# Performance work log

Hardware: AMD Instinct MI355X
Metric: run time of the kernel (lower is better)

Reference implementation:

```python
import jax, jax.numpy as jnp
import numpy as np

B = 2
H, W = 128, 128           # branch-0 map_size (target of all scatters)
N0 = 16384                # original grid points = H*W
IN_CH = [64, 128, 256, 512]
NS = [16384, 4096, 1024, 256]
OUT_C = 256
BN_EPS = 1e-5


def setup_inputs() -> dict:
    key = jax.random.key(0)
    ks = jax.random.split(key, 16)
    inp = {}
    for j, (c, n) in enumerate(zip(IN_CH, NS)):
        inp[f"x{j}"] = jax.random.normal(ks[4 * j], (B, n, c), jnp.float32)
        # grid_sample-style coords in [-1, 1]
        inp[f"loc{j}"] = jax.random.uniform(ks[4 * j + 1], (B, N0, 2), jnp.float32) * 2.0 - 1.0
        inp[f"idx{j}"] = jax.random.randint(ks[4 * j + 2], (B, N0), 0, n, dtype=jnp.int32)
        fan_out = 3 * 3 * OUT_C
        inp[f"w{j}"] = jax.random.normal(ks[4 * j + 3], (OUT_C, c, 3, 3), jnp.float32) * np.sqrt(2.0 / fan_out)
        inp[f"gamma{j}"] = jnp.ones((OUT_C,), jnp.float32)
        inp[f"beta{j}"] = jnp.zeros((OUT_C,), jnp.float32)
    return inp


def token2map(x, loc_orig, idx_agg):
    """Scatter-average token features x [B,N,C] onto a dense [B,C,H,W] map.
    Each of N0 original points carries the feature of its token (idx_agg) and
    lands in the grid cell given by loc_orig; cells average their points."""
    Bb, N, C = x.shape
    n0 = loc_orig.shape[1]
    loc = (jnp.clip(loc_orig, -1.0, 1.0) + 1.0) * 0.5
    ix = jnp.clip(jnp.round(loc[..., 0] * (W - 1)).astype(jnp.int32), 0, W - 1)
    iy = jnp.clip(jnp.round(loc[..., 1] * (H - 1)).astype(jnp.int32), 0, H - 1)
    cell = (ix + iy * W + jnp.arange(Bb, dtype=jnp.int32)[:, None] * (H * W)).reshape(-1)  # [B*N0]
    feat = jnp.take_along_axis(x, idx_agg[..., None], axis=1).reshape(Bb * n0, C)  # [B*N0, C]
    ones = jnp.ones((Bb * n0,), x.dtype)
    cnt = jax.ops.segment_sum(ones, cell, num_segments=Bb * H * W) + 1e-6  # points per cell
    val = (1.0 / cnt)[cell]  # per-point normalized weight
    out = jax.ops.segment_sum(feat * val[:, None], cell, num_segments=Bb * H * W)
    return out.reshape(Bb, H, W, C).transpose(0, 3, 1, 2)  # NCHW


def conv_bn(x, w, gamma, beta):
    # 3x3 stride-2 conv (bias=False) + BatchNorm2d (training mode: batch stats, biased var)
    y = jax.lax.conv_general_dilated(x, w, (2, 2), [(1, 1), (1, 1)],
                                     dimension_numbers=('NCHW', 'OIHW', 'NCHW'))
    mean = y.mean(axis=(0, 2, 3))
    var = y.var(axis=(0, 2, 3))
    y = (y - mean[None, :, None, None]) * jax.lax.rsqrt(var + BN_EPS)[None, :, None, None]
    return y * gamma[None, :, None, None] + beta[None, :, None, None]


def reference(x0, x1, x2, x3, loc0, loc1, loc2, loc3, idx0, idx1, idx2, idx3,
              w0, w1, w2, w3, gamma0, gamma1, gamma2, gamma3,
              beta0, beta1, beta2, beta3):
    xs = [x0, x1, x2, x3]
    locs = [loc0, loc1, loc2, loc3]
    idxs = [idx0, idx1, idx2, idx3]
    ws = [w0, w1, w2, w3]
    gs = [gamma0, gamma1, gamma2, gamma3]
    bs = [beta0, beta1, beta2, beta3]
    out_map = 0.0
    for j in range(4):  # fixed small loop over branches (structurally distinct C_j)
        m = token2map(xs[j], locs[j], idxs[j])
        out_map = out_map + conv_bn(m, ws[j], gs[j], bs[j])
    return out_map  # [B, 256, 64, 64]
```

## Files before the change

### kernel.cpp

```cpp
#include <hip/hip_runtime.h>

#define B 2
#define N0 16384
#define HW 16384
#define PADW 130
#define OUTC 256
#define M_ROWS 8192
#define MAXP 32

typedef short s16x8 __attribute__((ext_vector_type(8)));
typedef float f32x4 __attribute__((ext_vector_type(4)));

__device__ __forceinline__ unsigned short f2bf(float f) {
    union { float f; unsigned int u; } v; v.f = f;
    unsigned int u = v.u;
    return (unsigned short)((u + 0x7fffu + ((u >> 16) & 1u)) >> 16);
}
__device__ __forceinline__ float bf2f(unsigned short h) {
    union { unsigned int u; float f; } v; v.u = ((unsigned int)h) << 16;
    return v.f;
}

__device__ __forceinline__ void gl_lds16(const void* g, void* l) {
    __builtin_amdgcn_global_load_lds(
        (const __attribute__((address_space(1))) unsigned int*)g,
        (__attribute__((address_space(3))) unsigned int*)l, 16, 0, 0);
}

__device__ __forceinline__ void cell_of(const float* __restrict__ loc, int r, int& ix, int& iy) {
    float lx = loc[r * 2 + 0];
    float ly = loc[r * 2 + 1];
    lx = fminf(fmaxf(lx, -1.f), 1.f);
    ly = fminf(fmaxf(ly, -1.f), 1.f);
    ix = min(max((int)rintf(((lx + 1.f) * 0.5f) * 127.f), 0), 127);
    iy = min(max((int)rintf(((ly + 1.f) * 0.5f) * 127.f), 0), 127);
}

__global__ void fill_k(const float* __restrict__ l0, const float* __restrict__ l1,
                       const float* __restrict__ l2, const float* __restrict__ l3,
                       const int* __restrict__ i0, const int* __restrict__ i1,
                       const int* __restrict__ i2, const int* __restrict__ i3,
                       int* __restrict__ cnt32, unsigned short* __restrict__ list) {
    int p = blockIdx.x * 256 + threadIdx.x;
    int j = p >> 15, r = p & 32767;
    const float* loc = j == 0 ? l0 : j == 1 ? l1 : j == 2 ? l2 : l3;
    const int* idx = j == 0 ? i0 : j == 1 ? i1 : j == 2 ? i2 : i3;
    int ix, iy;
    cell_of(loc, r, ix, iy);
    int cidx = (((j << 1) + (r >> 14)) << 14) + iy * 128 + ix;
    int pos = atomicAdd(&cnt32[cidx], 1);
    if (pos < MAXP) list[cidx * MAXP + pos] = (unsigned short)idx[r];
}

__global__ void prep_k(const float* __restrict__ x0, const float* __restrict__ x1,
                       const float* __restrict__ x2, const float* __restrict__ x3,
                       const int* __restrict__ cnt32, const unsigned short* __restrict__ list,
                       unsigned short* __restrict__ mapB,
                       const float* __restrict__ w0, const float* __restrict__ w1,
                       const float* __restrict__ w2, const float* __restrict__ w3,
                       unsigned short* __restrict__ wt) {
    if (blockIdx.x >= 15844) {
        int i = (blockIdx.x - 15844) * 256 + threadIdx.x;
        if (i >= 2211840) return;
        int j, local;
        if (i < 147456) { j = 0; local = i; }
        else if (i < 442368) { j = 1; local = i - 147456; }
        else if (i < 1032192) { j = 2; local = i - 442368; }
        else { j = 3; local = i - 1032192; }
        const float* w = j == 0 ? w0 : j == 1 ? w1 : j == 2 ? w2 : w3;
        int lc = 6 + j, C = 1 << lc;
        int ci = local & (C - 1);
        int rest = local >> lc;
        int seg = rest % 9, co = rest / 9;
        int kh = seg / 3, kw = seg % 3;
        wt[(size_t)2304 * (C - 64) + local] = f2bf(w[(((co * C) + ci) * 3 + kh) * 3 + kw]);
        return;
    }
    int W = (blockIdx.x * 256 + threadIdx.x) >> 6;
    if (W >= 63375) return;
    int lane = threadIdx.x & 63;
    int j, base;
    if (W < 4225) { j = 0; base = 0; }
    else if (W < 12675) { j = 1; base = 4225; }
    else if (W < 29575) { j = 2; base = 12675; }
    else { j = 3; base = 29575; }
    const float* x = j == 0 ? x0 : j == 1 ? x1 : j == 2 ? x2 : x3;
    const int C = 64 << j;
    const int ntok = 16384 >> (2 * j);
    int u = W - base;
    int cellLocal = (u << (3 - j)) + (lane >> (3 + j));
    int sub = lane & ((8 << j) - 1);
    int ch0 = sub * 8;
    int b = cellLocal / 16900;
    int cc = cellLocal - b * 16900;
    int py = cc / 130, px = cc - py * 130;
    unsigned short* dst = mapB + (size_t)33800 * (C - 64) + ((size_t)cellLocal * C) + ch0;
    float a0 = 0.f, a1 = 0.f, a2 = 0.f, a3 = 0.f, a4 = 0.f, a5 = 0.f, a6 = 0.f, a7 = 0.f;
    if (py >= 1 && py <= 128 && px >= 1 && px <= 128) {
        int cidx = (((j << 1) + b) << 14) + (py - 1) * 128 + (px - 1);
        int n = cnt32[cidx];
        float inv = 1.0f / ((float)n + 1e-6f);
        int nn = min(n, MAXP);
        const unsigned short* lst = list + (size_t)cidx * MAXP;
        for (int p = 0; p < nn; p++) {
            int tok = lst[p];
            const float* xr = x + ((size_t)b * ntok + tok) * C + ch0;
            float4 v0 = *(const float4*)xr;
            float4 v1 = *(const float4*)(xr + 4);
            a0 += v0.x; a1 += v0.y; a2 += v0.z; a3 += v0.w;
            a4 += v1.x; a5 += v1.y; a6 += v1.z; a7 += v1.w;
        }
        a0 *= inv; a1 *= inv; a2 *= inv; a3 *= inv;
        a4 *= inv; a5 *= inv; a6 *= inv; a7 *= inv;
    }
    uint4 o;
    o.x = (unsigned int)f2bf(a0) | ((unsigned int)f2bf(a1) << 16);
    o.y = (unsigned int)f2bf(a2) | ((unsigned int)f2bf(a3) << 16);
    o.z = (unsigned int)f2bf(a4) | ((unsigned int)f2bf(a5) << 16);
    o.w = (unsigned int)f2bf(a6) | ((unsigned int)f2bf(a7) << 16);
    *(uint4*)dst = o;
}

__global__ __launch_bounds__(128) void conv_mfma(const unsigned short* __restrict__ mapB,
                                                 const unsigned short* __restrict__ wt,
                                                 unsigned short* __restrict__ P) {
    __shared__ unsigned short As[2][128][32];
    __shared__ unsigned short Bs[2][128][32];
    const int t = threadIdx.x;
    const int lane = t & 63;
    const int w = t >> 6;
    const int z = blockIdx.z;
    const int j = (z < 4) ? 3 : (z < 6) ? 2 : (z == 6) ? 1 : 0;
    const int lc = 6 + j;
    const int C = 1 << lc;
    const int K = 9 * C;
    const int s0 = (z < 4) ? z * 36 : (z == 5 ? 36 : 0);
    const int s1 = s0 + (j == 0 ? 18 : 36);
    const unsigned short* mapBj = mapB + (size_t)33800 * (C - 64);
    const unsigned short* wtj = wt + (size_t)2304 * (C - 64);
    unsigned short* Pz = P + (size_t)z * M_ROWS * OUTC;
    const int mt = blockIdx.x, nt = blockIdx.y;

    const int lr = lane >> 2, lq = lane & 3;
    const unsigned short* pA[4];
    const unsigned short* pB[4];
#pragma unroll
    for (int i = 0; i < 4; i++) {
        int r = w * 64 + i * 16 + lr;
        int s = mt * 128 + r;
        int b = s >> 12, rem = s & 4095, oh = rem >> 6, ow = rem & 63;
        pA[i] = mapBj + (size_t)((b * PADW + 2 * oh) * PADW + 2 * ow) * C + lq * 8;
        pB[i] = wtj + (size_t)(nt * 128 + r) * K + lq * 8;
    }

    int k0 = s0 << 5;
    int seg0 = k0 >> lc;
    int ci0 = k0 & (C - 1);
    int kh = seg0 / 3, kw = seg0 - 3 * kh;
    int offA = (kh * PADW + kw) * C + ci0;
    int offB = k0;

#pragma unroll
    for (int i = 0; i < 4; i++) {
        gl_lds16(pA[i] + offA, &As[0][w * 64 + i * 16][0]);
        gl_lds16(pB[i] + offB, &Bs[0][w * 64 + i * 16][0]);
    }

    f32x4 acc[8][4];
#pragma unroll
    for (int mi = 0; mi < 8; mi++)
#pragma unroll
        for (int ni = 0; ni < 4; ni++) acc[mi][ni] = (f32x4){0.f, 0.f, 0.f, 0.f};

    const int r16 = lane & 15, kg = lane >> 4;
    int buf = 0;
    for (int s = s0; s < s1; s++) {
        ci0 += 32; offA += 32; offB += 32;
        if (ci0 == C) {
            ci0 = 0; kw++;
            if (kw == 3) { kw = 0; offA += (PADW - 3) * C; }
        }
        __syncthreads();
        if (s + 1 < s1) {
            int nb = buf ^ 1;
#pragma unroll
            for (int i = 0; i < 4; i++) {
                gl_lds16(pA[i] + offA, &As[nb][w * 64 + i * 16][0]);
                gl_lds16(pB[i] + offB, &Bs[nb][w * 64 + i * 16][0]);
            }
        }
        s16x8 a[8], b[4];
#pragma unroll
        for (int mi = 0; mi < 8; mi++) a[mi] = *(const s16x8*)&As[buf][mi * 16 + r16][kg * 8];
#pragma unroll
        for (int ni = 0; ni < 4; ni++)
            b[ni] = *(const s16x8*)&Bs[buf][w * 64 + ni * 16 + r16][kg * 8];
#pragma unroll
        for (int mi = 0; mi < 8; mi++)
#pragma unroll
            for (int ni = 0; ni < 4; ni++)
                acc[mi][ni] = __builtin_amdgcn_mfma_f32_16x16x32_bf16(a[mi], b[ni],
                                                                      acc[mi][ni], 0, 0, 0);
        buf ^= 1;
    }

    const int rg = lane >> 4, c16 = lane & 15;
#pragma unroll
    for (int mi = 0; mi < 8; mi++)
#pragma unroll
        for (int ni = 0; ni < 4; ni++)
#pragma unroll
            for (int reg = 0; reg < 4; reg++) {
                int row = mt * 128 + mi * 16 + rg * 4 + reg;
                int col = nt * 128 + w * 64 + ni * 16 + c16;
                Pz[(size_t)row * OUTC + col] = f2bf(acc[mi][ni][reg]);
            }
}

__global__ void combine_k(const unsigned short* __restrict__ P,
                          unsigned short* __restrict__ ybr, float* __restrict__ branchAcc) {
    __shared__ float red_s[8][256], red_ss[8][256];
    int bi = blockIdx.x;
    int t = threadIdx.x;
    int cg = t & 31, rt = t >> 5;
    float s[4][8], ss[4][8];
#pragma unroll
    for (int j = 0; j < 4; j++)
#pragma unroll
        for (int k = 0; k < 8; k++) { s[j][k] = 0.f; ss[j][k] = 0.f; }
    for (int r = rt; r < 64; r += 8) {
        size_t row = (size_t)bi * 64 + r;
        const unsigned short* p = P + row * OUTC + cg * 8;
        float v[4][8];
#pragma unroll
        for (int j = 0; j < 4; j++)
#pragma unroll
            for (int k = 0; k < 8; k++) v[j][k] = 0.f;
#pragma unroll
        for (int z = 0; z < 8; z++) {
            int j = (z < 4) ? 3 : (z < 6) ? 2 : (z == 6) ? 1 : 0;
            uint4 u = *(const uint4*)(p + (size_t)z * M_ROWS * OUTC);
            v[j][0] += bf2f((unsigned short)(u.x & 0xffff));
            v[j][1] += bf2f((unsigned short)(u.x >> 16));
            v[j][2] += bf2f((unsigned short)(u.y & 0xffff));
            v[j][3] += bf2f((unsigned short)(u.y >> 16));
            v[j][4] += bf2f((unsigned short)(u.z & 0xffff));
            v[j][5] += bf2f((unsigned short)(u.z >> 16));
            v[j][6] += bf2f((unsigned short)(u.w & 0xffff));
            v[j][7] += bf2f((unsigned short)(u.w >> 16));
        }
#pragma unroll
        for (int j = 0; j < 4; j++) {
            uint4 o;
            o.x = (unsigned int)f2bf(v[j][0]) | ((unsigned int)f2bf(v[j][1]) << 16);
            o.y = (unsigned int)f2bf(v[j][2]) | ((unsigned int)f2bf(v[j][3]) << 16);
            o.z = (unsigned int)f2bf(v[j][4]) | ((unsigned int)f2bf(v[j][5]) << 16);
            o.w = (unsigned int)f2bf(v[j][6]) | ((unsigned int)f2bf(v[j][7]) << 16);
            *(uint4*)(ybr + ((size_t)j * M_ROWS + row) * OUTC + cg * 8) = o;
#pragma unroll
            for (int k = 0; k < 8; k++) {
                s[j][k] += v[j][k];
                ss[j][k] += v[j][k] * v[j][k];
            }
        }
    }
    for (int j = 0; j < 4; j++) {
#pragma unroll
        for (int k = 0; k < 8; k++) {
            red_s[rt][cg * 8 + k] = s[j][k];
            red_ss[rt][cg * 8 + k] = ss[j][k];
        }
        __syncthreads();
        float S = 0.f, SS = 0.f;
#pragma unroll
        for (int r = 0; r < 8; r++) { S += red_s[r][t]; SS += red_ss[r][t]; }
        atomicAdd(&branchAcc[j * 512 + t], S);
        atomicAdd(&branchAcc[j * 512 + 256 + t], SS);
        __syncthreads();
    }
}

__global__ void stats2_k(const float* __restrict__ branchAcc,
                         const float* __restrict__ g0, const float* __restrict__ g1,
                         const float* __restrict__ g2, const float* __restrict__ g3,
                         const float* __restrict__ b0, const float* __restrict__ b1,
                         const float* __restrict__ b2, const float* __restrict__ b3,
                         float* __restrict__ ssb) {
    int j = blockIdx.x, c = threadIdx.x;
    const float* gamma = j == 0 ? g0 : j == 1 ? g1 : j == 2 ? g2 : g3;
    const float* beta = j == 0 ? b0 : j == 1 ? b1 : j == 2 ? b2 : b3;
    float s = branchAcc[j * 512 + c];
    float ss = branchAcc[j * 512 + 256 + c];
    float mean = s * (1.f / 8192.f);
    float var = ss * (1.f / 8192.f) - mean * mean;
    float rs = rsqrtf(var + 1e-5f);
    float sc = gamma[c] * rs;
    ssb[j * 512 + c] = sc;
    ssb[j * 512 + OUTC + c] = beta[c] - mean * sc;
}

__global__ void out_k(const unsigned short* __restrict__ ybr, const float* __restrict__ ssb,
                      float* __restrict__ out) {
    __shared__ float tile[64][132];
    int oh = blockIdx.x, ct = blockIdx.y, b = blockIdx.z;
    int t = threadIdx.x;
    int cg = t & 31, rt = t >> 5;
    int c0 = ct * 128 + cg * 4;
    float sc[4][4], sh[4];
#pragma unroll
    for (int k = 0; k < 4; k++) {
        float shk = 0.f;
#pragma unroll
        for (int jj = 0; jj < 4; jj++) {
            sc[jj][k] = ssb[jj * 512 + c0 + k];
            shk += ssb[jj * 512 + OUTC + c0 + k];
        }
        sh[k] = shk;
    }
#pragma unroll
    for (int it = 0; it < 8; it++) {
        int ow = rt * 8 + it;
        size_t row = (size_t)b * 4096 + oh * 64 + ow;
        const unsigned short* p = ybr + row * OUTC + c0;
        float acc[4];
#pragma unroll
        for (int k = 0; k < 4; k++) acc[k] = sh[k];
#pragma unroll
        for (int jj = 0; jj < 4; jj++) {
            ushort4 u = *(const ushort4*)(p + (size_t)jj * M_ROWS * OUTC);
            acc[0] += bf2f(u.x) * sc[jj][0];
            acc[1] += bf2f(u.y) * sc[jj][1];
            acc[2] += bf2f(u.z) * sc[jj][2];
            acc[3] += bf2f(u.w) * sc[jj][3];
        }
#pragma unroll
        for (int k = 0; k < 4; k++) tile[ow][cg * 4 + k] = acc[k];
    }
    __syncthreads();
    int owq = t & 15, cp = t >> 4;
#pragma unroll
    for (int pass = 0; pass < 8; pass++) {
        int c = pass * 16 + cp;
        float4 v;
        v.x = tile[owq * 4 + 0][c];
        v.y = tile[owq * 4 + 1][c];
        v.z = tile[owq * 4 + 2][c];
        v.w = tile[owq * 4 + 3][c];
        *(float4*)(out + (((size_t)b * OUTC + ct * 128 + c) * 64 + oh) * 64 + owq * 4) = v;
    }
}

extern "C" void kernel_launch(void* const* d_in, const int* in_sizes, int n_in,
                              void* d_out, int out_size, void* d_ws, size_t ws_size,
                              hipStream_t stream) {
    char* ws = (char*)d_ws;
    size_t off = 0;
    auto alloc = [&](size_t bytes) {
        void* p = ws + off;
        off = (off + bytes + 255) & ~(size_t)255;
        return p;
    };
    unsigned short* P = (unsigned short*)alloc((size_t)8 * M_ROWS * OUTC * 2);
    unsigned short* wt = (unsigned short*)alloc((size_t)2304 * 960 * 2);
    unsigned short* mapB = (unsigned short*)alloc((size_t)33800 * 960 * 2);
    unsigned short* ybr = mapB;
    int* cnt32 = (int*)alloc((size_t)4 * 2 * HW * 4);
    float* branchAcc = (float*)alloc((size_t)4 * 512 * 4);
    unsigned short* list = (unsigned short*)alloc((size_t)4 * 2 * HW * MAXP * 2);
    float* ssb = (float*)alloc((size_t)4 * 512 * 4);

    hipMemsetAsync(cnt32, 0, (size_t)4 * 2 * HW * 4 + 4 * 512 * 4, stream);

    fill_k<<<512, 256, 0, stream>>>(
        (const float*)d_in[1], (const float*)d_in[7], (const float*)d_in[13],
        (const float*)d_in[19],
        (const int*)d_in[2], (const int*)d_in[8], (const int*)d_in[14],
        (const int*)d_in[20], cnt32, list);
    prep_k<<<15844 + 8640, 256, 0, stream>>>(
        (const float*)d_in[0], (const float*)d_in[6], (const float*)d_in[12],
        (const float*)d_in[18], cnt32, list, mapB,
        (const float*)d_in[3], (const float*)d_in[9], (const float*)d_in[15],
        (const float*)d_in[21], wt);
    conv_mfma<<<dim3(64, 2, 8), 128, 0, stream>>>(mapB, wt, P);
    combine_k<<<128, 256, 0, stream>>>(P, ybr, branchAcc);
    stats2_k<<<4, 256, 0, stream>>>(branchAcc,
        (const float*)d_in[4], (const float*)d_in[10], (const float*)d_in[16],
        (const float*)d_in[22],
        (const float*)d_in[5], (const float*)d_in[11], (const float*)d_in[17],
        (const float*)d_in[23], ssb);
    out_k<<<dim3(64, 2, 2), 256, 0, stream>>>(ybr, ssb, (float*)d_out);
}
```

Measured before the change: 242.5 us.

## Use 4-wave conv tiles with register B loads; fuse BN finalize into output

The conv kernel moves to 256 threads in a 2x2 wave layout, each wave computing 64x64. Only A is staged through LDS; the weight fragments are loaded straight from global into registers, and the K loop is unrolled by two with ping-pong buffers. The combine kernel no longer writes per-branch bf16 intermediates, and only computes the BN statistics, now over twice as many blocks. The stats finalize kernel is folded into out_k, which rereads all 8 partial slices of P. This drops two launches and the ybr round trip, at the cost of extra reads in out_k and uncoalesced direct global B loads in the conv.

```diff
diff --git a/kernel.cpp b/kernel.cpp
--- a/kernel.cpp
+++ b/kernel.cpp
@@ -121,14 +121,14 @@
     *(uint4*)dst = o;
 }
 
-__global__ __launch_bounds__(128) void conv_mfma(const unsigned short* __restrict__ mapB,
+__global__ __launch_bounds__(256) void conv_mfma(const unsigned short* __restrict__ mapB,
                                                  const unsigned short* __restrict__ wt,
                                                  unsigned short* __restrict__ P) {
     __shared__ unsigned short As[2][128][32];
-    __shared__ unsigned short Bs[2][128][32];
     const int t = threadIdx.x;
     const int lane = t & 63;
     const int w = t >> 6;
+    const int wm = w >> 1, wn = w & 1;
     const int z = blockIdx.z;
     const int j = (z < 4) ? 3 : (z < 6) ? 2 : (z == 6) ? 1 : 0;
     const int lc = 6 + j;
@@ -142,83 +142,103 @@
     const int mt = blockIdx.x, nt = blockIdx.y;
 
     const int lr = lane >> 2, lq = lane & 3;
-    const unsigned short* pA[4];
-    const unsigned short* pB[4];
-#pragma unroll
-    for (int i = 0; i < 4; i++) {
-        int r = w * 64 + i * 16 + lr;
+    const unsigned short* pA[2];
+#pragma unroll
+    for (int i = 0; i < 2; i++) {
+        int r = w * 32 + i * 16 + lr;
         int s = mt * 128 + r;
         int b = s >> 12, rem = s & 4095, oh = rem >> 6, ow = rem & 63;
         pA[i] = mapBj + (size_t)((b * PADW + 2 * oh) * PADW + 2 * ow) * C + lq * 8;
-        pB[i] = wtj + (size_t)(nt * 128 + r) * K + lq * 8;
-    }
+    }
+
+    const int r16 = lane & 15, kg = lane >> 4;
+    const unsigned short* pBrow[4];
+#pragma unroll
+    for (int ni = 0; ni < 4; ni++)
+        pBrow[ni] = wtj + (size_t)(nt * 128 + wn * 64 + ni * 16 + r16) * K + kg * 8;
 
     int k0 = s0 << 5;
+    int ci0 = k0 & (C - 1);
     int seg0 = k0 >> lc;
-    int ci0 = k0 & (C - 1);
     int kh = seg0 / 3, kw = seg0 - 3 * kh;
     int offA = (kh * PADW + kw) * C + ci0;
     int offB = k0;
 
-#pragma unroll
-    for (int i = 0; i < 4; i++) {
-        gl_lds16(pA[i] + offA, &As[0][w * 64 + i * 16][0]);
-        gl_lds16(pB[i] + offB, &Bs[0][w * 64 + i * 16][0]);
-    }
-
-    f32x4 acc[8][4];
-#pragma unroll
-    for (int mi = 0; mi < 8; mi++)
+    gl_lds16(pA[0] + offA, &As[0][w * 32][0]);
+    gl_lds16(pA[1] + offA, &As[0][w * 32 + 16][0]);
+    s16x8 bA[4], bB[4];
+#pragma unroll
+    for (int ni = 0; ni < 4; ni++) bA[ni] = *(const s16x8*)(pBrow[ni] + offB);
+
+    f32x4 acc[4][4];
+#pragma unroll
+    for (int mi = 0; mi < 4; mi++)
 #pragma unroll
         for (int ni = 0; ni < 4; ni++) acc[mi][ni] = (f32x4){0.f, 0.f, 0.f, 0.f};
 
-    const int r16 = lane & 15, kg = lane >> 4;
-    int buf = 0;
-    for (int s = s0; s < s1; s++) {
-        ci0 += 32; offA += 32; offB += 32;
-        if (ci0 == C) {
-            ci0 = 0; kw++;
-            if (kw == 3) { kw = 0; offA += (PADW - 3) * C; }
-        }
+#define ADVANCE() do { ci0 += 32; offA += 32; offB += 32; \
+        if (ci0 == C) { ci0 = 0; kw++; if (kw == 3) { kw = 0; offA += (PADW - 3) * C; } } } while (0)
+
+#define COMPUTE(BUF, BREG) do { \
+        s16x8 a0 = *(const s16x8*)&As[BUF][wm * 64 + 0 * 16 + r16][kg * 8]; \
+        s16x8 a1 = *(const s16x8*)&As[BUF][wm * 64 + 1 * 16 + r16][kg * 8]; \
+        s16x8 a2 = *(const s16x8*)&As[BUF][wm * 64 + 2 * 16 + r16][kg * 8]; \
+        s16x8 a3 = *(const s16x8*)&As[BUF][wm * 64 + 3 * 16 + r16][kg * 8]; \
+        acc[0][0] = __builtin_amdgcn_mfma_f32_16x16x32_bf16(a0, BREG[0], acc[0][0], 0, 0, 0); \
+        acc[0][1] = __builtin_amdgcn_mfma_f32_16x16x32_bf16(a0, BREG[1], acc[0][1], 0, 0, 0); \
+        acc[0][2] = __builtin_amdgcn_mfma_f32_16x16x32_bf16(a0, BREG[2], acc[0][2], 0, 0, 0); \
+        acc[0][3] = __builtin_amdgcn_mfma_f32_16x16x32_bf16(a0, BREG[3], acc[0][3], 0, 0, 0); \
+        acc[1][0] = __builtin_amdgcn_mfma_f32_16x16x32_bf16(a1, BREG[0], acc[1][0], 0, 0, 0); \
+        acc[1][1] = __builtin_amdgcn_mfma_f32_16x16x32_bf16(a1, BREG[1], acc[1][1], 0, 0, 0); \
+        acc[1][2] = __builtin_amdgcn_mfma_f32_16x16x32_bf16(a1, BREG[2], acc[1][2], 0, 0, 0); \
+        acc[1][3] = __builtin_amdgcn_mfma_f32_16x16x32_bf16(a1, BREG[3], acc[1][3], 0, 0, 0); \
+        acc[2][0] = __builtin_amdgcn_mfma_f32_16x16x32_bf16(a2, BREG[0], acc[2][0], 0, 0, 0); \
+        acc[2][1] = __builtin_amdgcn_mfma_f32_16x16x32_bf16(a2, BREG[1], acc[2][1], 0, 0, 0); \
+        acc[2][2] = __builtin_amdgcn_mfma_f32_16x16x32_bf16(a2, BREG[2], acc[2][2], 0, 0, 0); \
+        acc[2][3] = __builtin_amdgcn_mfma_f32_16x16x32_bf16(a2, BREG[3], acc[2][3], 0, 0, 0); \
+        acc[3][0] = __builtin_amdgcn_mfma_f32_16x16x32_bf16(a3, BREG[0], acc[3][0], 0, 0, 0); \
+        acc[3][1] = __builtin_amdgcn_mfma_f32_16x16x32_bf16(a3, BREG[1], acc[3][1], 0, 0, 0); \
+        acc[3][2] = __builtin_amdgcn_mfma_f32_16x16x32_bf16(a3, BREG[2], acc[3][2], 0, 0, 0); \
+        acc[3][3] = __builtin_amdgcn_mfma_f32_16x16x32_bf16(a3, BREG[3], acc[3][3], 0, 0, 0); \
+    } while (0)
+
+    for (int s = s0; s < s1; s += 2) {
+        ADVANCE();
         __syncthreads();
         if (s + 1 < s1) {
-            int nb = buf ^ 1;
-#pragma unroll
-            for (int i = 0; i < 4; i++) {
-                gl_lds16(pA[i] + offA, &As[nb][w * 64 + i * 16][0]);
-                gl_lds16(pB[i] + offB, &Bs[nb][w * 64 + i * 16][0]);
-            }
-        }
-        s16x8 a[8], b[4];
-#pragma unroll
-        for (int mi = 0; mi < 8; mi++) a[mi] = *(const s16x8*)&As[buf][mi * 16 + r16][kg * 8];
+            gl_lds16(pA[0] + offA, &As[1][w * 32][0]);
+            gl_lds16(pA[1] + offA, &As[1][w * 32 + 16][0]);
+#pragma unroll
+            for (int ni = 0; ni < 4; ni++) bB[ni] = *(const s16x8*)(pBrow[ni] + offB);
+        }
+        COMPUTE(0, bA);
+        ADVANCE();
+        __syncthreads();
+        if (s + 2 < s1) {
+            gl_lds16(pA[0] + offA, &As[0][w * 32][0]);
+            gl_lds16(pA[1] + offA, &As[0][w * 32 + 16][0]);
+#pragma unroll
+            for (int ni = 0; ni < 4; ni++) bA[ni] = *(const s16x8*)(pBrow[ni] + offB);
+        }
+        COMPUTE(1, bB);
+    }
+#undef ADVANCE
+#undef COMPUTE
+
+    const int rg = lane >> 4, c16 = lane & 15;
+#pragma unroll
+    for (int mi = 0; mi < 4; mi++)
 #pragma unroll
         for (int ni = 0; ni < 4; ni++)
-            b[ni] = *(const s16x8*)&Bs[buf][w * 64 + ni * 16 + r16][kg * 8];
-#pragma unroll
-        for (int mi = 0; mi < 8; mi++)
-#pragma unroll
-            for (int ni = 0; ni < 4; ni++)
-                acc[mi][ni] = __builtin_amdgcn_mfma_f32_16x16x32_bf16(a[mi], b[ni],
-                                                                      acc[mi][ni], 0, 0, 0);
-        buf ^= 1;
-    }
-
-    const int rg = lane >> 4, c16 = lane & 15;
-#pragma unroll
-    for (int mi = 0; mi < 8; mi++)
-#pragma unroll
-        for (int ni = 0; ni < 4; ni++)
 #pragma unroll
             for (int reg = 0; reg < 4; reg++) {
-                int row = mt * 128 + mi * 16 + rg * 4 + reg;
-                int col = nt * 128 + w * 64 + ni * 16 + c16;
+                int row = mt * 128 + wm * 64 + mi * 16 + rg * 4 + reg;
+                int col = nt * 128 + wn * 64 + ni * 16 + c16;
                 Pz[(size_t)row * OUTC + col] = f2bf(acc[mi][ni][reg]);
             }
 }
 
-__global__ void combine_k(const unsigned short* __restrict__ P,
-                          unsigned short* __restrict__ ybr, float* __restrict__ branchAcc) {
+__global__ void statsC_k(const unsigned short* __restrict__ P, float* __restrict__ branchAcc) {
     __shared__ float red_s[8][256], red_ss[8][256];
     int bi = blockIdx.x;
     int t = threadIdx.x;
@@ -228,8 +248,8 @@
     for (int j = 0; j < 4; j++)
 #pragma unroll
         for (int k = 0; k < 8; k++) { s[j][k] = 0.f; ss[j][k] = 0.f; }
-    for (int r = rt; r < 64; r += 8) {
-        size_t row = (size_t)bi * 64 + r;
+    for (int r = rt; r < 32; r += 8) {
+        size_t row = (size_t)bi * 32 + r;
         const unsigned short* p = P + row * OUTC + cg * 8;
         float v[4][8];
 #pragma unroll
@@ -237,9 +257,9 @@
 #pragma unroll
             for (int k = 0; k < 8; k++) v[j][k] = 0.f;
 #pragma unroll
-        for (int z = 0; z < 8; z++) {
-            int j = (z < 4) ? 3 : (z < 6) ? 2 : (z == 6) ? 1 : 0;
-            uint4 u = *(const uint4*)(p + (size_t)z * M_ROWS * OUTC);
+        for (int zz = 0; zz < 8; zz++) {
+            int j = (zz < 4) ? 3 : (zz < 6) ? 2 : (zz == 6) ? 1 : 0;
+            uint4 u = *(const uint4*)(p + (size_t)zz * M_ROWS * OUTC);
             v[j][0] += bf2f((unsigned short)(u.x & 0xffff));
             v[j][1] += bf2f((unsigned short)(u.x >> 16));
             v[j][2] += bf2f((unsigned short)(u.y & 0xffff));
@@ -250,19 +270,12 @@
             v[j][7] += bf2f((unsigned short)(u.w >> 16));
         }
 #pragma unroll
-        for (int j = 0; j < 4; j++) {
-            uint4 o;
-            o.x = (unsigned int)f2bf(v[j][0]) | ((unsigned int)f2bf(v[j][1]) << 16);
-            o.y = (unsigned int)f2bf(v[j][2]) | ((unsigned int)f2bf(v[j][3]) << 16);
-            o.z = (unsigned int)f2bf(v[j][4]) | ((unsigned int)f2bf(v[j][5]) << 16);
-            o.w = (unsigned int)f2bf(v[j][6]) | ((unsigned int)f2bf(v[j][7]) << 16);
-            *(uint4*)(ybr + ((size_t)j * M_ROWS + row) * OUTC + cg * 8) = o;
+        for (int j = 0; j < 4; j++)
 #pragma unroll
             for (int k = 0; k < 8; k++) {
                 s[j][k] += v[j][k];
                 ss[j][k] += v[j][k] * v[j][k];
             }
-        }
     }
     for (int j = 0; j < 4; j++) {
 #pragma unroll
@@ -280,26 +293,11 @@
     }
 }
 
-__global__ void stats2_k(const float* __restrict__ branchAcc,
-                         const float* __restrict__ g0, const float* __restrict__ g1,
-                         const float* __restrict__ g2, const float* __restrict__ g3,
-                         const float* __restrict__ b0, const float* __restrict__ b1,
-                         const float* __restrict__ b2, const float* __restrict__ b3,
-                         float* __restrict__ ssb) {
-    int j = blockIdx.x, c = threadIdx.x;
-    const float* gamma = j == 0 ? g0 : j == 1 ? g1 : j == 2 ? g2 : g3;
-    const float* beta = j == 0 ? b0 : j == 1 ? b1 : j == 2 ? b2 : b3;
-    float s = branchAcc[j * 512 + c];
-    float ss = branchAcc[j * 512 + 256 + c];
-    float mean = s * (1.f / 8192.f);
-    float var = ss * (1.f / 8192.f) - mean * mean;
-    float rs = rsqrtf(var + 1e-5f);
-    float sc = gamma[c] * rs;
-    ssb[j * 512 + c] = sc;
-    ssb[j * 512 + OUTC + c] = beta[c] - mean * sc;
-}
-
-__global__ void out_k(const unsigned short* __restrict__ ybr, const float* __restrict__ ssb,
+__global__ void out_k(const unsigned short* __restrict__ P, const float* __restrict__ branchAcc,
+                      const float* __restrict__ g0, const float* __restrict__ g1,
+                      const float* __restrict__ g2, const float* __restrict__ g3,
+                      const float* __restrict__ b0, const float* __restrict__ b1,
+                      const float* __restrict__ b2, const float* __restrict__ b3,
                       float* __restrict__ out) {
     __shared__ float tile[64][132];
     int oh = blockIdx.x, ct = blockIdx.y, b = blockIdx.z;
@@ -309,11 +307,20 @@
     float sc[4][4], sh[4];
 #pragma unroll
     for (int k = 0; k < 4; k++) {
+        int c = c0 + k;
         float shk = 0.f;
 #pragma unroll
         for (int jj = 0; jj < 4; jj++) {
-            sc[jj][k] = ssb[jj * 512 + c0 + k];
-            shk += ssb[jj * 512 + OUTC + c0 + k];
+            const float* gamma = jj == 0 ? g0 : jj == 1 ? g1 : jj == 2 ? g2 : g3;
+            const float* beta = jj == 0 ? b0 : jj == 1 ? b1 : jj == 2 ? b2 : b3;
+            float sum = branchAcc[jj * 512 + c];
+            float sumsq = branchAcc[jj * 512 + 256 + c];
+            float mean = sum * (1.f / 8192.f);
+            float var = sumsq * (1.f / 8192.f) - mean * mean;
+            float rs = rsqrtf(var + 1e-5f);
+            float scv = gamma[c] * rs;
+            sc[jj][k] = scv;
+            shk += beta[c] - mean * scv;
         }
         sh[k] = shk;
     }
@@ -321,20 +328,23 @@
     for (int it = 0; it < 8; it++) {
         int ow = rt * 8 + it;
         size_t row = (size_t)b * 4096 + oh * 64 + ow;
-        const unsigned short* p = ybr + row * OUTC + c0;
-        float acc[4];
-#pragma unroll
-        for (int k = 0; k < 4; k++) acc[k] = sh[k];
-#pragma unroll
-        for (int jj = 0; jj < 4; jj++) {
-            ushort4 u = *(const ushort4*)(p + (size_t)jj * M_ROWS * OUTC);
-            acc[0] += bf2f(u.x) * sc[jj][0];
-            acc[1] += bf2f(u.y) * sc[jj][1];
-            acc[2] += bf2f(u.z) * sc[jj][2];
-            acc[3] += bf2f(u.w) * sc[jj][3];
-        }
-#pragma unroll
-        for (int k = 0; k < 4; k++) tile[ow][cg * 4 + k] = acc[k];
+        const unsigned short* p = P + row * OUTC + c0;
+        float a3k[4], a2k[4], a1k[4], a0k[4];
+#pragma unroll
+        for (int k = 0; k < 4; k++) { a3k[k] = a2k[k] = a1k[k] = a0k[k] = 0.f; }
+#pragma unroll
+        for (int zz = 0; zz < 8; zz++) {
+            ushort4 u = *(const ushort4*)(p + (size_t)zz * M_ROWS * OUTC);
+            float* a = zz < 4 ? a3k : zz < 6 ? a2k : (zz == 6 ? a1k : a0k);
+            a[0] += bf2f(u.x);
+            a[1] += bf2f(u.y);
+            a[2] += bf2f(u.z);
+            a[3] += bf2f(u.w);
+        }
+#pragma unroll
+        for (int k = 0; k < 4; k++)
+            tile[ow][cg * 4 + k] = sh[k] + a3k[k] * sc[3][k] + a2k[k] * sc[2][k] +
+                                   a1k[k] * sc[1][k] + a0k[k] * sc[0][k];
     }
     __syncthreads();
     int owq = t & 15, cp = t >> 4;
@@ -363,11 +373,9 @@
     unsigned short* P = (unsigned short*)alloc((size_t)8 * M_ROWS * OUTC * 2);
     unsigned short* wt = (unsigned short*)alloc((size_t)2304 * 960 * 2);
     unsigned short* mapB = (unsigned short*)alloc((size_t)33800 * 960 * 2);
-    unsigned short* ybr = mapB;
     int* cnt32 = (int*)alloc((size_t)4 * 2 * HW * 4);
     float* branchAcc = (float*)alloc((size_t)4 * 512 * 4);
     unsigned short* list = (unsigned short*)alloc((size_t)4 * 2 * HW * MAXP * 2);
-    float* ssb = (float*)alloc((size_t)4 * 512 * 4);
 
     hipMemsetAsync(cnt32, 0, (size_t)4 * 2 * HW * 4 + 4 * 512 * 4, stream);
 
@@ -381,12 +389,11 @@
         (const float*)d_in[18], cnt32, list, mapB,
         (const float*)d_in[3], (const float*)d_in[9], (const float*)d_in[15],
         (const float*)d_in[21], wt);
-    conv_mfma<<<dim3(64, 2, 8), 128, 0, stream>>>(mapB, wt, P);
-    combine_k<<<128, 256, 0, stream>>>(P, ybr, branchAcc);
-    stats2_k<<<4, 256, 0, stream>>>(branchAcc,
+    conv_mfma<<<dim3(64, 2, 8), 256, 0, stream>>>(mapB, wt, P);
+    statsC_k<<<256, 256, 0, stream>>>(P, branchAcc);
+    out_k<<<dim3(64, 2, 2), 256, 0, stream>>>(P, branchAcc,
         (const float*)d_in[4], (const float*)d_in[10], (const float*)d_in[16],
         (const float*)d_in[22],
         (const float*)d_in[5], (const float*)d_in[11], (const float*)d_in[17],
-        (const float*)d_in[23], ssb);
-    out_k<<<dim3(64, 2, 2), 256, 0, stream>>>(ybr, ssb, (float*)d_out);
-}
+        (const float*)d_in[23], (float*)d_out);
+}
```

Measured after the change: 256.8 us. 5.9% more time.
